# Optimization experiments

Measured on AMD Instinct MI355X. Metric: run time of the kernel, lower is better.

The kernel has to match this reference:

```python
import jax, jax.numpy as jnp
import numpy as np

EMBED_DIM = 1024
NUM_HEADS = 16
D_K = EMBED_DIM // NUM_HEADS


def setup_inputs() -> dict:
    key = jax.random.key(0)
    kx, kq, kk, kv, ko = jax.random.split(key, 5)
    scale = 1.0 / np.sqrt(EMBED_DIM)
    x = jax.random.normal(kx, (4, 2048, EMBED_DIM), dtype=jnp.float32)
    # Linear(embed_dim, embed_dim, bias=False) weights, stored [out, in] like torch
    Wq = jax.random.uniform(kq, (EMBED_DIM, EMBED_DIM), jnp.float32, -scale, scale)
    Wk = jax.random.uniform(kk, (EMBED_DIM, EMBED_DIM), jnp.float32, -scale, scale)
    Wv = jax.random.uniform(kv, (EMBED_DIM, EMBED_DIM), jnp.float32, -scale, scale)
    Wo = jax.random.uniform(ko, (EMBED_DIM, EMBED_DIM), jnp.float32, -scale, scale)
    return {"x": x, "Wq": Wq, "Wk": Wk, "Wv": Wv, "Wo": Wo}


def reference(x, Wq, Wk, Wv, Wo):
    b, s, _ = x.shape
    # torch Linear: y = x @ W.T
    def proj(W):
        y = jnp.einsum('bse,fe->bsf', x, W)
        return y.reshape(b, s, NUM_HEADS, D_K).transpose(0, 2, 1, 3)  # [b,h,s,d]
    q, k, v = proj(Wq), proj(Wk), proj(Wv)
    scores = jnp.einsum('bhqd,bhkd->bhqk', q, k) / jnp.sqrt(jnp.float32(D_K))
    attn = jax.nn.softmax(scores, axis=-1)  # dropout is identity in eval
    out = jnp.einsum('bhqk,bhkd->bhqd', attn, v)
    out = out.transpose(0, 2, 1, 3).reshape(b, s, EMBED_DIM)
    return jnp.einsum('bsf,ef->bse', out, Wo)
```

## Files before the change

kernel.cpp:

```cpp
#include <hip/hip_runtime.h>
#include <hip/hip_bf16.h>

typedef unsigned short u16;
typedef unsigned int   u32;
typedef __attribute__((ext_vector_type(8))) __bf16 bf16x8;
typedef __attribute__((ext_vector_type(2))) __bf16 bf16x2;
typedef __attribute__((ext_vector_type(8))) u16    ushort8v;
typedef __attribute__((ext_vector_type(2))) float  f32x2;
typedef __attribute__((ext_vector_type(4))) float  floatx4;

#define EMBED 1024
#define SEQ   2048
#define BATCH 4
#define NH    16
#define DKH   64
#define BHN   (BATCH*NH)
#define ZSTRIDE ((size_t)BHN*SEQ*DKH)

__device__ __forceinline__ u16 f2bf(float f){
  union { float f; unsigned u; } v; v.f = f;
  unsigned r = (v.u + 0x7FFFu + ((v.u >> 16) & 1u)) >> 16;
  return (u16)r;
}
__device__ __forceinline__ u32 pk2(float a, float b){
  f32x2 v = {a, b};
  return __builtin_bit_cast(u32, __builtin_convertvector(v, bf16x2));
}

__device__ __forceinline__ bf16x8 ld_frag(const u16* p){
  return __builtin_bit_cast(bf16x8, *(const ushort8v*)p);
}

__device__ __forceinline__ floatx4 mfma16(bf16x8 a, bf16x8 b, floatx4 c){
  return __builtin_amdgcn_mfma_f32_16x16x32_bf16(a, b, c, 0, 0, 0);
}

__device__ __forceinline__ void gl_lds16(const u16* g, u16* l){
  __builtin_amdgcn_global_load_lds((const __attribute__((address_space(1))) void*)g,
                                   (__attribute__((address_space(3))) void*)l,
                                   16, 0, 0);
}

__global__ __launch_bounds__(256) void cvt_all(const float* __restrict__ x,
    const float* __restrict__ wq, const float* __restrict__ wk,
    const float* __restrict__ wv, const float* __restrict__ wo,
    u16* __restrict__ Xb, u16* __restrict__ Wqb, u16* __restrict__ Wkb,
    u16* __restrict__ Wvb, u16* __restrict__ Wob){
  int b = blockIdx.x;
  const float* src; u16* dst; int i;
  if (b < 8192){ src = x; dst = Xb; i = b*256 + threadIdx.x; }
  else {
    int k = (b - 8192) >> 10, r = (b - 8192) & 1023;
    src = (k==0) ? wq : (k==1) ? wk : (k==2) ? wv : wo;
    dst = (k==0) ? Wqb : (k==1) ? Wkb : (k==2) ? Wvb : Wob;
    i = r*256 + threadIdx.x;
  }
  float4 v = ((const float4*)src)[i];
  ushort4 o;
  o.x = f2bf(v.x); o.y = f2bf(v.y); o.z = f2bf(v.z); o.w = f2bf(v.w);
  ((ushort4*)dst)[i] = o;
}

__device__ __forceinline__ void gemm_core_db(const u16* Abase, const u16* Bbase,
                                             u16* As, u16* Bs, floatx4 acc[4][4]){
  const int tid  = threadIdx.x;
  const int lane = tid & 63, w = tid >> 6;
  const int lm   = lane & 15, quad = lane >> 4;
  const int wm   = (w & 1) * 64, wn = (w >> 1) * 64;
  const int row0 = tid >> 2, kc = tid & 3;
  const int row1 = (256 + tid) >> 2;

  #pragma unroll
  for (int mi = 0; mi < 4; ++mi)
    #pragma unroll
    for (int ni = 0; ni < 4; ++ni)
      acc[mi][ni] = (floatx4){0.f, 0.f, 0.f, 0.f};

  gl_lds16(Abase + (size_t)row0*EMBED + kc*8, As + tid*8);
  gl_lds16(Bbase + (size_t)row0*EMBED + kc*8, Bs + tid*8);
  gl_lds16(Abase + (size_t)row1*EMBED + kc*8, As + (256 + tid)*8);
  gl_lds16(Bbase + (size_t)row1*EMBED + kc*8, Bs + (256 + tid)*8);

  for (int kt = 0; kt < EMBED/32; ++kt){
    const int cur = kt & 1;
    __syncthreads();
    if (kt + 1 < EMBED/32){
      const int k0 = (kt + 1) * 32;
      u16* Ad = As + (cur^1)*128*32;
      u16* Bd = Bs + (cur^1)*128*32;
      gl_lds16(Abase + (size_t)row0*EMBED + k0 + kc*8, Ad + tid*8);
      gl_lds16(Bbase + (size_t)row0*EMBED + k0 + kc*8, Bd + tid*8);
      gl_lds16(Abase + (size_t)row1*EMBED + k0 + kc*8, Ad + (256 + tid)*8);
      gl_lds16(Bbase + (size_t)row1*EMBED + k0 + kc*8, Bd + (256 + tid)*8);
    }
    const u16* Ac = As + cur*128*32;
    const u16* Bc = Bs + cur*128*32;
    bf16x8 af[4], bf[4];
    #pragma unroll
    for (int mi = 0; mi < 4; ++mi)
      af[mi] = ld_frag(&Ac[(wm + mi*16 + lm)*32 + quad*8]);
    #pragma unroll
    for (int ni = 0; ni < 4; ++ni)
      bf[ni] = ld_frag(&Bc[(wn + ni*16 + lm)*32 + quad*8]);
    #pragma unroll
    for (int mi = 0; mi < 4; ++mi)
      #pragma unroll
      for (int ni = 0; ni < 4; ++ni)
        acc[mi][ni] = mfma16(af[mi], bf[ni], acc[mi][ni]);
  }
}

#define QSCALE 0.1803368801111204f
__global__ __launch_bounds__(256) void gemm_qkv(const u16* __restrict__ X,
    const u16* __restrict__ Wq, const u16* __restrict__ Wk, const u16* __restrict__ Wv,
    u16* __restrict__ QKV){
  __shared__ __attribute__((aligned(16))) u16 As[2*128*32];
  __shared__ __attribute__((aligned(16))) u16 Bs[2*128*32];
  const int z  = blockIdx.y >> 3;
  const u16* W = (z == 0) ? Wq : (z == 1) ? Wk : Wv;
  const int m0 = blockIdx.x * 128, n0 = (blockIdx.y & 7) * 128;
  floatx4 acc[4][4];
  gemm_core_db(X + (size_t)m0*EMBED, W + (size_t)n0*EMBED, As, Bs, acc);

  const int tid = threadIdx.x, lane = tid & 63, w = tid >> 6;
  const int lm = lane & 15, quad = lane >> 4;
  const int wm = (w & 1) * 64, wn = (w >> 1) * 64;
  u16* outz = QKV + (size_t)z * ZSTRIDE;

  if (z == 2){
    #pragma unroll
    for (int mi = 0; mi < 4; ++mi)
      #pragma unroll
      for (int ni = 0; ni < 4; ++ni){
        int mbase = m0 + wm + mi*16 + quad*4;
        int n = n0 + wn + ni*16 + lm;
        int b = mbase >> 11, sb = mbase & 2047;
        int h = n >> 6, d = n & 63;
        u16* dst = outz + (((size_t)(b*NH + h))*DKH + d)*SEQ + sb;
        uint2 pv;
        pv.x = pk2(acc[mi][ni][0], acc[mi][ni][1]);
        pv.y = pk2(acc[mi][ni][2], acc[mi][ni][3]);
        *reinterpret_cast<uint2*>(dst) = pv;
      }
  } else {
    const float scale = (z == 0) ? QSCALE : 1.0f;
    #pragma unroll
    for (int mi = 0; mi < 4; ++mi)
      #pragma unroll
      for (int ni = 0; ni < 4; ++ni)
        #pragma unroll
        for (int r = 0; r < 4; ++r){
          int m = m0 + wm + mi*16 + quad*4 + r;
          int n = n0 + wn + ni*16 + lm;
          int b = m >> 11, s = m & 2047, h = n >> 6, d = n & 63;
          outz[(((size_t)(b*NH + h))*SEQ + s)*DKH + d] = f2bf(acc[mi][ni][r] * scale);
        }
  }
}

__global__ __launch_bounds__(256) void gemm_out(const u16* __restrict__ A,
    const u16* __restrict__ W, float* __restrict__ C){
  __shared__ __attribute__((aligned(16))) u16 As[2*128*32];
  __shared__ __attribute__((aligned(16))) u16 Bs[2*128*32];
  const int m0 = blockIdx.x * 128, n0 = blockIdx.y * 128;
  floatx4 acc[4][4];
  gemm_core_db(A + (size_t)m0*EMBED, W + (size_t)n0*EMBED, As, Bs, acc);

  const int tid = threadIdx.x, lane = tid & 63, w = tid >> 6;
  const int lm = lane & 15, quad = lane >> 4;
  const int wm = (w & 1) * 64, wn = (w >> 1) * 64;
  #pragma unroll
  for (int mi = 0; mi < 4; ++mi)
    #pragma unroll
    for (int ni = 0; ni < 4; ++ni)
      #pragma unroll
      for (int r = 0; r < 4; ++r){
        int m = m0 + wm + mi*16 + quad*4 + r;
        int n = n0 + wn + ni*16 + lm;
        C[(size_t)m*EMBED + n] = acc[mi][ni][r];
      }
}

#define KSS 520
__global__ __launch_bounds__(256, 4) void attn_kernel(const u16* __restrict__ QKV,
                                                      u16* __restrict__ Out){
  __shared__ __attribute__((aligned(16))) u16 Ks[2][8*KSS];
  __shared__ __attribute__((aligned(16))) u16 Vs[2][64*64];

  const int tid = threadIdx.x, lane = tid & 63, w = tid >> 6;
  const int lm = lane & 15, quad = lane >> 4;
  const int bh = blockIdx.x;
  const int q0 = blockIdx.y * 128;
  const u16* Qh = QKV + (size_t)bh * SEQ * DKH;
  const u16* Kh = QKV + ZSTRIDE + (size_t)bh * SEQ * DKH;
  const u16* Vh = QKV + 2*ZSTRIDE + (size_t)bh * DKH * SEQ;

  const int sK = tid & 63, cK = tid >> 6;
  const int dV = tid >> 3, gV = tid & 7;
  const size_t vsrc0 = (size_t)dV * SEQ + ((gV ^ (dV & 7)) * 8);
  const size_t vsrc1 = vsrc0 + (size_t)32 * SEQ;

  bf16x8 qf[2][2];
  #pragma unroll
  for (int qt = 0; qt < 2; ++qt)
    #pragma unroll
    for (int st = 0; st < 2; ++st)
      qf[qt][st] = ld_frag(Qh + (size_t)(q0 + w*32 + qt*16 + lm)*DKH + st*32 + quad*8);

  const uint4 ONESW = {0x3F803F80u, 0x3F803F80u, 0x3F803F80u, 0x3F803F80u};
  const bf16x8 ones8 = __builtin_bit_cast(bf16x8, ONESW);

  floatx4 o[2][4], lac[2];
  #pragma unroll
  for (int qt = 0; qt < 2; ++qt){
    lac[qt] = (floatx4){0.f, 0.f, 0.f, 0.f};
    #pragma unroll
    for (int dt = 0; dt < 4; ++dt) o[qt][dt] = (floatx4){0.f, 0.f, 0.f, 0.f};
  }

  gl_lds16(Kh + (size_t)sK*DKH + cK*8,     Ks[0] + cK*KSS + sK*8);
  gl_lds16(Kh + (size_t)sK*DKH + (cK+4)*8, Ks[0] + (cK+4)*KSS + sK*8);
  gl_lds16(Vh + vsrc0,                     Vs[0] + tid*8);
  gl_lds16(Vh + vsrc1,                     Vs[0] + 2048 + tid*8);

  for (int kt = 0; kt < SEQ/64; ++kt){
    const int cur = kt & 1;
    __syncthreads();
    if (kt + 1 < SEQ/64){
      const int nk0 = (kt + 1) * 64;
      gl_lds16(Kh + (size_t)(nk0 + sK)*DKH + cK*8,     Ks[cur^1] + cK*KSS + sK*8);
      gl_lds16(Kh + (size_t)(nk0 + sK)*DKH + (cK+4)*8, Ks[cur^1] + (cK+4)*KSS + sK*8);
      gl_lds16(Vh + vsrc0 + nk0,                       Vs[cur^1] + tid*8);
      gl_lds16(Vh + vsrc1 + nk0,                       Vs[cur^1] + 2048 + tid*8);
    }
    const u16* Kc = Ks[cur];
    const u16* Vc = Vs[cur];

    #pragma unroll
    for (int u = 0; u < 2; ++u){
      uint2 ph[2][2];
      #pragma unroll
      for (int half = 0; half < 2; ++half){
        const int t = u*2 + half;
        bf16x8 kf0 = ld_frag(&Kc[quad*KSS     + (t*16 + lm)*8]);
        bf16x8 kf1 = ld_frag(&Kc[(quad+4)*KSS + (t*16 + lm)*8]);
        #pragma unroll
        for (int qt = 0; qt < 2; ++qt){
          floatx4 s = (floatx4){0.f,0.f,0.f,0.f};
          s = mfma16(kf0, qf[qt][0], s);
          s = mfma16(kf1, qf[qt][1], s);
          ph[qt][half].x = pk2(__builtin_amdgcn_exp2f(s[0]), __builtin_amdgcn_exp2f(s[1]));
          ph[qt][half].y = pk2(__builtin_amdgcn_exp2f(s[2]), __builtin_amdgcn_exp2f(s[3]));
        }
      }
      bf16x8 pf[2];
      #pragma unroll
      for (int qt = 0; qt < 2; ++qt){
        uint4 pp = {ph[qt][0].x, ph[qt][0].y, ph[qt][1].x, ph[qt][1].y};
        pf[qt] = __builtin_bit_cast(bf16x8, pp);
      }
      lac[0] = mfma16(pf[0], ones8, lac[0]);
      lac[1] = mfma16(pf[1], ones8, lac[1]);
      const int cg0 = (((u*4     + (quad >> 1)) ^ (lm & 7)) * 8) + (quad & 1) * 4;
      const int cg1 = (((u*4 + 2 + (quad >> 1)) ^ (lm & 7)) * 8) + (quad & 1) * 4;
      #pragma unroll
      for (int dt = 0; dt < 4; ++dt){
        uint2 vlo = *(const uint2*)(Vc + (dt*16 + lm)*64 + cg0);
        uint2 vhi = *(const uint2*)(Vc + (dt*16 + lm)*64 + cg1);
        uint4 vv = {vlo.x, vlo.y, vhi.x, vhi.y};
        bf16x8 vb = __builtin_bit_cast(bf16x8, vv);
        o[0][dt] = mfma16(pf[0], vb, o[0][dt]);
        o[1][dt] = mfma16(pf[1], vb, o[1][dt]);
      }
    }
  }

  const int bI = bh >> 4, h = bh & 15;
  #pragma unroll
  for (int qt = 0; qt < 2; ++qt){
    floatx4 inv;
    #pragma unroll
    for (int r = 0; r < 4; ++r) inv[r] = __builtin_amdgcn_rcpf(lac[qt][r]);
    #pragma unroll
    for (int dt = 0; dt < 4; ++dt)
      #pragma unroll
      for (int r = 0; r < 4; ++r){
        int s = q0 + w*32 + qt*16 + quad*4 + r;
        Out[((size_t)(bI*SEQ + s))*EMBED + h*DKH + dt*16 + lm] = f2bf(o[qt][dt][r] * inv[r]);
      }
  }
}

extern "C" void kernel_launch(void* const* d_in, const int* in_sizes, int n_in,
                              void* d_out, int out_size, void* d_ws, size_t ws_size,
                              hipStream_t stream){
  const float* x  = (const float*)d_in[0];
  const float* Wq = (const float*)d_in[1];
  const float* Wk = (const float*)d_in[2];
  const float* Wv = (const float*)d_in[3];
  const float* Wo = (const float*)d_in[4];
  float* out = (float*)d_out;

  char* ws = (char*)d_ws;
  u16* Xb  = (u16*)ws;
  u16* Wqb = (u16*)(ws + (size_t)16777216);
  u16* Wkb = Wqb + 1048576;
  u16* Wvb = Wkb + 1048576;
  u16* Wob = Wvb + 1048576;
  u16* QKV = (u16*)(ws + (size_t)25165824);
  u16* At  = (u16*)(ws + (size_t)75497472);

  cvt_all<<<12288, 256, 0, stream>>>(x, Wq, Wk, Wv, Wo, Xb, Wqb, Wkb, Wvb, Wob);
  gemm_qkv<<<dim3(64, 24), 256, 0, stream>>>(Xb, Wqb, Wkb, Wvb, QKV);
  attn_kernel<<<dim3(64, 16), 256, 0, stream>>>(QKV, At);
  gemm_out<<<dim3(64, 8), 256, 0, stream>>>(At, Wob, out);
}
```

Baseline: 272.1 us.

## Stage Q/K epilogue through LDS for vector stores; raise MFMA wave priority

The Q/K epilogue of the QKV projection GEMM now writes the bf16 results into a padded shared-memory tile, two 64-column halves at a time. It then issues 16-byte vectorized global stores instead of scattered 2-byte per-element stores. The A/B LDS buffers are merged into one array so the tile can reuse that space, which adds extra barriers. Separately, the attention inner loop wraps its MFMA sections in s_setprio(1)/s_setprio(0) so waves doing matrix math get issue priority over waves doing exp and loads.

```diff
diff --git a/kernel.cpp b/kernel.cpp
--- a/kernel.cpp
+++ b/kernel.cpp
@@ -114,8 +114,9 @@
 __global__ __launch_bounds__(256) void gemm_qkv(const u16* __restrict__ X,
     const u16* __restrict__ Wq, const u16* __restrict__ Wk, const u16* __restrict__ Wv,
     u16* __restrict__ QKV){
-  __shared__ __attribute__((aligned(16))) u16 As[2*128*32];
-  __shared__ __attribute__((aligned(16))) u16 Bs[2*128*32];
+  __shared__ __attribute__((aligned(16))) u16 SM[4*128*32];
+  u16* As = SM;
+  u16* Bs = SM + 2*128*32;
   const int z  = blockIdx.y >> 3;
   const u16* W = (z == 0) ? Wq : (z == 1) ? Wk : Wv;
   const int m0 = blockIdx.x * 128, n0 = (blockIdx.y & 7) * 128;
@@ -144,17 +145,37 @@
       }
   } else {
     const float scale = (z == 0) ? QSCALE : 1.0f;
-    #pragma unroll
-    for (int mi = 0; mi < 4; ++mi)
-      #pragma unroll
-      for (int ni = 0; ni < 4; ++ni)
+    u16* T = SM;
+    __syncthreads();
+    #pragma unroll
+    for (int p = 0; p < 2; ++p){
+      if ((w >> 1) == p){
         #pragma unroll
-        for (int r = 0; r < 4; ++r){
-          int m = m0 + wm + mi*16 + quad*4 + r;
-          int n = n0 + wn + ni*16 + lm;
-          int b = m >> 11, s = m & 2047, h = n >> 6, d = n & 63;
-          outz[(((size_t)(b*NH + h))*SEQ + s)*DKH + d] = f2bf(acc[mi][ni][r] * scale);
+        for (int mi = 0; mi < 4; ++mi)
+          #pragma unroll
+          for (int ni = 0; ni < 4; ++ni){
+            const int mb = wm + mi*16 + quad*4;
+            const int nn = ni*16 + lm;
+            #pragma unroll
+            for (int r = 0; r < 4; ++r)
+              T[(mb + r)*72 + nn] = f2bf(acc[mi][ni][r] * scale);
+          }
+      }
+      __syncthreads();
+      {
+        const int ml = tid >> 1, nh = (tid & 1) * 32;
+        const int mg = m0 + ml, b = mg >> 11, s = mg & 2047;
+        #pragma unroll
+        for (int j = 0; j < 4; ++j){
+          const int nl = nh + j*8;
+          const int n = n0 + p*64 + nl;
+          const int h = n >> 6, d = n & 63;
+          *(ushort8v*)(outz + (((size_t)(b*NH + h))*SEQ + s)*DKH + d) =
+              *(const ushort8v*)&T[(size_t)ml*72 + nl];
         }
+      }
+      if (p == 0) __syncthreads();
+    }
   }
 }
 
@@ -247,8 +268,10 @@
         #pragma unroll
         for (int qt = 0; qt < 2; ++qt){
           floatx4 s = (floatx4){0.f,0.f,0.f,0.f};
+          __builtin_amdgcn_s_setprio(1);
           s = mfma16(kf0, qf[qt][0], s);
           s = mfma16(kf1, qf[qt][1], s);
+          __builtin_amdgcn_s_setprio(0);
           ph[qt][half].x = pk2(__builtin_amdgcn_exp2f(s[0]), __builtin_amdgcn_exp2f(s[1]));
           ph[qt][half].y = pk2(__builtin_amdgcn_exp2f(s[2]), __builtin_amdgcn_exp2f(s[3]));
         }
@@ -259,10 +282,11 @@
         uint4 pp = {ph[qt][0].x, ph[qt][0].y, ph[qt][1].x, ph[qt][1].y};
         pf[qt] = __builtin_bit_cast(bf16x8, pp);
       }
+      const int cg0 = (((u*4     + (quad >> 1)) ^ (lm & 7)) * 8) + (quad & 1) * 4;
+      const int cg1 = (((u*4 + 2 + (quad >> 1)) ^ (lm & 7)) * 8) + (quad & 1) * 4;
+      __builtin_amdgcn_s_setprio(1);
       lac[0] = mfma16(pf[0], ones8, lac[0]);
       lac[1] = mfma16(pf[1], ones8, lac[1]);
-      const int cg0 = (((u*4     + (quad >> 1)) ^ (lm & 7)) * 8) + (quad & 1) * 4;
-      const int cg1 = (((u*4 + 2 + (quad >> 1)) ^ (lm & 7)) * 8) + (quad & 1) * 4;
       #pragma unroll
       for (int dt = 0; dt < 4; ++dt){
         uint2 vlo = *(const uint2*)(Vc + (dt*16 + lm)*64 + cg0);
@@ -272,6 +296,7 @@
         o[0][dt] = mfma16(pf[0], vb, o[0][dt]);
         o[1][dt] = mfma16(pf[1], vb, o[1][dt]);
       }
+      __builtin_amdgcn_s_setprio(0);
     }
   }
 
```

Measured after the change: 273.2 us. No clear change (+0.4%).

## Fuse Q/K/V projections per block to share X tiles; prioritize attention MFMAs

Applied to the files above, without the earlier changes.

The QKV GEMM now has each block compute the Q, K and V outputs for the same 128x128 tile. Each loaded X tile is reused against three weight tiles, which cuts redundant A-operand loads and shrinks the grid from 1536 to 512 blocks. The cost is three times the accumulator registers (192 floats per lane), higher LDS use and fewer blocks, which risks lower occupancy and spills despite the launch_bounds hint. Separately, the attention kernel wraps its MFMA sections in s_setprio to favour matrix-issue waves.

```diff
diff --git a/kernel.cpp b/kernel.cpp
--- a/kernel.cpp
+++ b/kernel.cpp
@@ -111,23 +111,92 @@
 }
 
 #define QSCALE 0.1803368801111204f
-__global__ __launch_bounds__(256) void gemm_qkv(const u16* __restrict__ X,
+__global__ __launch_bounds__(256, 2) void gemm_qkv(const u16* __restrict__ X,
     const u16* __restrict__ Wq, const u16* __restrict__ Wk, const u16* __restrict__ Wv,
     u16* __restrict__ QKV){
   __shared__ __attribute__((aligned(16))) u16 As[2*128*32];
-  __shared__ __attribute__((aligned(16))) u16 Bs[2*128*32];
-  const int z  = blockIdx.y >> 3;
-  const u16* W = (z == 0) ? Wq : (z == 1) ? Wk : Wv;
-  const int m0 = blockIdx.x * 128, n0 = (blockIdx.y & 7) * 128;
-  floatx4 acc[4][4];
-  gemm_core_db(X + (size_t)m0*EMBED, W + (size_t)n0*EMBED, As, Bs, acc);
+  __shared__ __attribute__((aligned(16))) u16 Bs[3][2*128*32];
 
   const int tid = threadIdx.x, lane = tid & 63, w = tid >> 6;
   const int lm = lane & 15, quad = lane >> 4;
   const int wm = (w & 1) * 64, wn = (w >> 1) * 64;
-  u16* outz = QKV + (size_t)z * ZSTRIDE;
-
-  if (z == 2){
+  const int m0 = blockIdx.x * 128, n0 = blockIdx.y * 128;
+  const int row0 = tid >> 2, kc = tid & 3;
+
+  const u16* A0 = X  + (size_t)(m0 + row0)*EMBED + kc*8;
+  const u16* B0[3] = {
+    Wq + (size_t)(n0 + row0)*EMBED + kc*8,
+    Wk + (size_t)(n0 + row0)*EMBED + kc*8,
+    Wv + (size_t)(n0 + row0)*EMBED + kc*8 };
+
+  floatx4 acc[3][4][4];
+  #pragma unroll
+  for (int z = 0; z < 3; ++z)
+    #pragma unroll
+    for (int mi = 0; mi < 4; ++mi)
+      #pragma unroll
+      for (int ni = 0; ni < 4; ++ni)
+        acc[z][mi][ni] = (floatx4){0.f, 0.f, 0.f, 0.f};
+
+  gl_lds16(A0,             As + tid*8);
+  gl_lds16(A0 + 64*EMBED,  As + (256 + tid)*8);
+  #pragma unroll
+  for (int z = 0; z < 3; ++z){
+    gl_lds16(B0[z],            Bs[z] + tid*8);
+    gl_lds16(B0[z] + 64*EMBED, Bs[z] + (256 + tid)*8);
+  }
+
+  for (int kt = 0; kt < EMBED/32; ++kt){
+    const int cur = kt & 1;
+    __syncthreads();
+    if (kt + 1 < EMBED/32){
+      const int k0 = (kt + 1) * 32;
+      gl_lds16(A0 + k0,            As + (cur^1)*4096 + tid*8);
+      gl_lds16(A0 + 64*EMBED + k0, As + (cur^1)*4096 + (256 + tid)*8);
+      #pragma unroll
+      for (int z = 0; z < 3; ++z){
+        gl_lds16(B0[z] + k0,            Bs[z] + (cur^1)*4096 + tid*8);
+        gl_lds16(B0[z] + 64*EMBED + k0, Bs[z] + (cur^1)*4096 + (256 + tid)*8);
+      }
+    }
+    const u16* Ac = As + cur*4096;
+    bf16x8 af[4];
+    #pragma unroll
+    for (int mi = 0; mi < 4; ++mi)
+      af[mi] = ld_frag(&Ac[(wm + mi*16 + lm)*32 + quad*8]);
+    #pragma unroll
+    for (int z = 0; z < 3; ++z){
+      const u16* Bc = Bs[z] + cur*4096;
+      bf16x8 bfz[4];
+      #pragma unroll
+      for (int ni = 0; ni < 4; ++ni)
+        bfz[ni] = ld_frag(&Bc[(wn + ni*16 + lm)*32 + quad*8]);
+      #pragma unroll
+      for (int mi = 0; mi < 4; ++mi)
+        #pragma unroll
+        for (int ni = 0; ni < 4; ++ni)
+          acc[z][mi][ni] = mfma16(af[mi], bfz[ni], acc[z][mi][ni]);
+    }
+  }
+
+  #pragma unroll
+  for (int z = 0; z < 2; ++z){
+    const float scale = (z == 0) ? QSCALE : 1.0f;
+    u16* outz = QKV + (size_t)z * ZSTRIDE;
+    #pragma unroll
+    for (int mi = 0; mi < 4; ++mi)
+      #pragma unroll
+      for (int ni = 0; ni < 4; ++ni)
+        #pragma unroll
+        for (int r = 0; r < 4; ++r){
+          int m = m0 + wm + mi*16 + quad*4 + r;
+          int n = n0 + wn + ni*16 + lm;
+          int b = m >> 11, s = m & 2047, h = n >> 6, d = n & 63;
+          outz[(((size_t)(b*NH + h))*SEQ + s)*DKH + d] = f2bf(acc[z][mi][ni][r] * scale);
+        }
+  }
+  {
+    u16* outz = QKV + (size_t)2 * ZSTRIDE;
     #pragma unroll
     for (int mi = 0; mi < 4; ++mi)
       #pragma unroll
@@ -138,23 +207,10 @@
         int h = n >> 6, d = n & 63;
         u16* dst = outz + (((size_t)(b*NH + h))*DKH + d)*SEQ + sb;
         uint2 pv;
-        pv.x = pk2(acc[mi][ni][0], acc[mi][ni][1]);
-        pv.y = pk2(acc[mi][ni][2], acc[mi][ni][3]);
+        pv.x = pk2(acc[2][mi][ni][0], acc[2][mi][ni][1]);
+        pv.y = pk2(acc[2][mi][ni][2], acc[2][mi][ni][3]);
         *reinterpret_cast<uint2*>(dst) = pv;
       }
-  } else {
-    const float scale = (z == 0) ? QSCALE : 1.0f;
-    #pragma unroll
-    for (int mi = 0; mi < 4; ++mi)
-      #pragma unroll
-      for (int ni = 0; ni < 4; ++ni)
-        #pragma unroll
-        for (int r = 0; r < 4; ++r){
-          int m = m0 + wm + mi*16 + quad*4 + r;
-          int n = n0 + wn + ni*16 + lm;
-          int b = m >> 11, s = m & 2047, h = n >> 6, d = n & 63;
-          outz[(((size_t)(b*NH + h))*SEQ + s)*DKH + d] = f2bf(acc[mi][ni][r] * scale);
-        }
   }
 }
 
@@ -247,8 +303,10 @@
         #pragma unroll
         for (int qt = 0; qt < 2; ++qt){
           floatx4 s = (floatx4){0.f,0.f,0.f,0.f};
+          __builtin_amdgcn_s_setprio(1);
           s = mfma16(kf0, qf[qt][0], s);
           s = mfma16(kf1, qf[qt][1], s);
+          __builtin_amdgcn_s_setprio(0);
           ph[qt][half].x = pk2(__builtin_amdgcn_exp2f(s[0]), __builtin_amdgcn_exp2f(s[1]));
           ph[qt][half].y = pk2(__builtin_amdgcn_exp2f(s[2]), __builtin_amdgcn_exp2f(s[3]));
         }
@@ -259,10 +317,11 @@
         uint4 pp = {ph[qt][0].x, ph[qt][0].y, ph[qt][1].x, ph[qt][1].y};
         pf[qt] = __builtin_bit_cast(bf16x8, pp);
       }
+      const int cg0 = (((u*4     + (quad >> 1)) ^ (lm & 7)) * 8) + (quad & 1) * 4;
+      const int cg1 = (((u*4 + 2 + (quad >> 1)) ^ (lm & 7)) * 8) + (quad & 1) * 4;
+      __builtin_amdgcn_s_setprio(1);
       lac[0] = mfma16(pf[0], ones8, lac[0]);
       lac[1] = mfma16(pf[1], ones8, lac[1]);
-      const int cg0 = (((u*4     + (quad >> 1)) ^ (lm & 7)) * 8) + (quad & 1) * 4;
-      const int cg1 = (((u*4 + 2 + (quad >> 1)) ^ (lm & 7)) * 8) + (quad & 1) * 4;
       #pragma unroll
       for (int dt = 0; dt < 4; ++dt){
         uint2 vlo = *(const uint2*)(Vc + (dt*16 + lm)*64 + cg0);
@@ -272,6 +331,7 @@
         o[0][dt] = mfma16(pf[0], vb, o[0][dt]);
         o[1][dt] = mfma16(pf[1], vb, o[1][dt]);
       }
+      __builtin_amdgcn_s_setprio(0);
     }
   }
 
@@ -311,7 +371,7 @@
   u16* At  = (u16*)(ws + (size_t)75497472);
 
   cvt_all<<<12288, 256, 0, stream>>>(x, Wq, Wk, Wv, Wo, Xb, Wqb, Wkb, Wvb, Wob);
-  gemm_qkv<<<dim3(64, 24), 256, 0, stream>>>(Xb, Wqb, Wkb, Wvb, QKV);
+  gemm_qkv<<<dim3(64, 8), 256, 0, stream>>>(Xb, Wqb, Wkb, Wvb, QKV);
   attn_kernel<<<dim3(64, 16), 256, 0, stream>>>(QKV, At);
   gemm_out<<<dim3(64, 8), 256, 0, stream>>>(At, Wob, out);
 }
```

Measured after the change: 253.1 us. 7.0% less time.
